# Optimization experiments

Measured on AMD Instinct MI355X. Metric: run time of the kernel, lower is better.

Reference implementation:

```python
import jax, jax.numpy as jnp
import numpy as np

B, T, D = 4, 2048, 1024
H, S = 16, 64  # n_heads, stalk_dim; D == H*S
P_ADIC_BASE = 2
MAX_VAL = 16


def quantize_6bit(x):
    # symmetric int6 quantization with straight-through estimator
    scale = jnp.max(jnp.abs(x)) / 31.0 + 1e-8
    q = jnp.clip(jnp.round(x / scale), -31, 31) * scale
    return x + jax.lax.stop_gradient(q - x)


def build_p_adic_bias(seq_len, p=2, max_val=16):
    idx = jnp.arange(seq_len)
    d = jnp.abs(idx[:, None] - idx[None, :])
    nonzero = d > 0
    vp = jnp.zeros_like(d)
    work = d
    for _ in range(max_val):  # fixed iterations; v_2(|i-j|) <= log2(T) < 16
        divisible = nonzero & (work % p == 0)
        vp = vp + divisible.astype(vp.dtype)
        work = jnp.where(divisible, work // p, work)
    vals = jnp.minimum(vp, max_val).astype(jnp.float32)
    vals = jnp.where(nonzero, vals, jnp.float32(max_val))
    return vals / max_val


def setup_inputs() -> dict:
    key = jax.random.key(0)
    ks = jax.random.split(key, 8)
    std = 0.02
    return {
        "x": jax.random.normal(ks[0], (B, T, D), dtype=jnp.float32),
        "wq": jax.random.normal(ks[1], (D, D), dtype=jnp.float32) * std,
        "wk": jax.random.normal(ks[2], (D, D), dtype=jnp.float32) * std,
        "wv": jax.random.normal(ks[3], (D, D), dtype=jnp.float32) * std,
        "wo": jax.random.normal(ks[4], (D, D), dtype=jnp.float32) * std,
        "wu": jax.random.normal(ks[5], (S, S), dtype=jnp.float32) * std,
        "wsv": jax.random.normal(ks[6], (S, S), dtype=jnp.float32) * std,
        "p_scale": jnp.ones((1,), dtype=jnp.float32) * 0.1,
    }


def reference(x, wq, wk, wv, wo, wu, wsv, p_scale):
    h, s = H, S
    scale = 1.0 / jnp.sqrt(jnp.float32(s))
    # quantized linear projections (F.linear: x @ W.T)
    Q = (x @ quantize_6bit(wq).T).reshape(B, T, h, s).transpose(0, 2, 1, 3)
    K = (x @ quantize_6bit(wk).T).reshape(B, T, h, s).transpose(0, 2, 1, 3)
    V = (x @ quantize_6bit(wv).T).reshape(B, T, h, s).transpose(0, 2, 1, 3)
    # stalk (low-rank sheaf) maps on the head dim
    Qs = Q @ quantize_6bit(wu).T
    Ks = K @ quantize_6bit(wsv).T
    scores = jnp.einsum("bhqs,bhks->bhqk", Qs, Ks) * scale
    p_bias = build_p_adic_bias(T, p=P_ADIC_BASE, max_val=MAX_VAL)
    scores = scores + p_scale[0] * p_bias[None, None, :, :]
    causal = jnp.triu(jnp.ones((T, T), dtype=bool), k=1)
    scores = jnp.where(causal[None, None], -jnp.inf, scores)
    attn = jax.nn.softmax(scores, axis=-1)
    out = jnp.einsum("bhqk,bhks->bhqs", attn, V)
    out = out.transpose(0, 2, 1, 3).reshape(B, T, D)
    return out @ quantize_6bit(wo).T
```

## Files before the change

### kernel.cpp

```cpp
#include <hip/hip_runtime.h>
#include <hip/hip_bf16.h>
#include <stdint.h>


typedef __bf16 bf16_t;
typedef __attribute__((ext_vector_type(4))) __bf16 bf16x4;
typedef __attribute__((ext_vector_type(8))) __bf16 bf16x8;
typedef __attribute__((ext_vector_type(4))) float f32x4;

#define BB 4
#define TT 2048
#define DD 1024
#define HH 16
#define SS 64

__device__ __forceinline__ float quant6(float v, float s) {
    float q = rintf(v / s);
    q = fminf(fmaxf(q, -31.0f), 31.0f);
    return q * s;
}

__device__ __forceinline__ float fexp2(float x) {
#if __has_builtin(__builtin_amdgcn_exp2f)
    return __builtin_amdgcn_exp2f(x);
#else
    return exp2f(x);
#endif
}

typedef __attribute__((address_space(3))) uint32_t lds_u32;
typedef const __attribute__((address_space(1))) uint32_t glb_u32;

__global__ __launch_bounds__(256) void absmax6(const float* __restrict__ wq,
                                               const float* __restrict__ wk,
                                               const float* __restrict__ wv,
                                               const float* __restrict__ wo,
                                               const float* __restrict__ wu,
                                               const float* __restrict__ wsv,
                                               float* __restrict__ amax) {
    const int t = blockIdx.y;
    const float* src = (t == 0) ? wq : (t == 1) ? wk : (t == 2) ? wv
                     : (t == 3) ? wo : (t == 4) ? wu : wsv;
    const int n4 = (t < 4) ? (1048576 / 4) : (4096 / 4);
    float m = 0.0f;
    for (int i = blockIdx.x * blockDim.x + threadIdx.x; i < n4; i += gridDim.x * blockDim.x) {
        float4 v = ((const float4*)src)[i];
        m = fmaxf(m, fmaxf(fmaxf(fabsf(v.x), fabsf(v.y)), fmaxf(fabsf(v.z), fabsf(v.w))));
    }
    #pragma unroll
    for (int mask = 32; mask > 0; mask >>= 1)
        m = fmaxf(m, __shfl_xor(m, mask));
    __shared__ float red[4];
    int w = threadIdx.x >> 6;
    if ((threadIdx.x & 63) == 0) red[w] = m;
    __syncthreads();
    if (threadIdx.x == 0) {
        m = fmaxf(fmaxf(red[0], red[1]), fmaxf(red[2], red[3]));
        atomicMax((int*)(amax + t), __float_as_int(m));
    }
}

__global__ __launch_bounds__(256) void xcvt_kernel(const float* __restrict__ x,
                                                   bf16_t* __restrict__ xb) {
    int i = (blockIdx.x * 256 + threadIdx.x) * 8;
    float4 f0 = *(const float4*)(x + i);
    float4 f1 = *(const float4*)(x + i + 4);
    bf16x8 v;
    v[0] = (bf16_t)f0.x; v[1] = (bf16_t)f0.y; v[2] = (bf16_t)f0.z; v[3] = (bf16_t)f0.w;
    v[4] = (bf16_t)f1.x; v[5] = (bf16_t)f1.y; v[6] = (bf16_t)f1.z; v[7] = (bf16_t)f1.w;
    *(bf16x8*)(xb + i) = v;
}

__global__ __launch_bounds__(256) void prep_w(const float* __restrict__ wq,
                                              const float* __restrict__ wk,
                                              const float* __restrict__ wv,
                                              const float* __restrict__ wo,
                                              const float* __restrict__ wu,
                                              const float* __restrict__ wsv,
                                              const float* __restrict__ amax,
                                              bf16_t* __restrict__ W_all,
                                              bf16_t* __restrict__ Wo) {
    const int which = blockIdx.y;
    if (blockIdx.x < 512) {
        const float* src = which ? wo : wv;
        bf16_t* dst = which ? Wo : (W_all + (size_t)2048 * 1024);
        float s = amax[which ? 3 : 2] / 31.0f + 1e-8f;
        int i = (blockIdx.x * 256 + threadIdx.x) * 8;
        float4 f0 = *(const float4*)(src + i);
        float4 f1 = *(const float4*)(src + i + 4);
        bf16x8 v;
        v[0] = (bf16_t)quant6(f0.x, s); v[1] = (bf16_t)quant6(f0.y, s);
        v[2] = (bf16_t)quant6(f0.z, s); v[3] = (bf16_t)quant6(f0.w, s);
        v[4] = (bf16_t)quant6(f1.x, s); v[5] = (bf16_t)quant6(f1.y, s);
        v[6] = (bf16_t)quant6(f1.z, s); v[7] = (bf16_t)quant6(f1.w, s);
        *(bf16x8*)(dst + i) = v;
        return;
    }
    const int fx = blockIdx.x - 512;
    const float* wbig = which ? wk : wq;
    const float* wsml = which ? wsv : wu;
    const float sb = amax[which ? 1 : 0] / 31.0f + 1e-8f;
    const float ss = amax[which ? 5 : 4] / 31.0f + 1e-8f;
    const float oscale = which ? 1.0f : 0.125f * 1.44269504089f;
    bf16_t* outp = W_all + (size_t)which * 1024 * 1024;
    const int h = fx >> 4, n0 = (fx & 15) * 64;
    const int w = threadIdx.x >> 6, l = threadIdx.x & 63;
    const int l15 = l & 15, quad = l >> 4, q8 = quad * 8;
    const int m0 = w * 16;

    bf16x8 af[2];
    #pragma unroll
    for (int kc = 0; kc < 2; ++kc) {
        const float* src = wsml + (m0 + l15) * 64 + kc * 32 + q8;
        float4 f0 = *(const float4*)(src);
        float4 f1 = *(const float4*)(src + 4);
        bf16x8 a;
        a[0] = (bf16_t)quant6(f0.x, ss); a[1] = (bf16_t)quant6(f0.y, ss);
        a[2] = (bf16_t)quant6(f0.z, ss); a[3] = (bf16_t)quant6(f0.w, ss);
        a[4] = (bf16_t)quant6(f1.x, ss); a[5] = (bf16_t)quant6(f1.y, ss);
        a[6] = (bf16_t)quant6(f1.z, ss); a[7] = (bf16_t)quant6(f1.w, ss);
        af[kc] = a;
    }
    f32x4 acc[4];
    #pragma unroll
    for (int nb = 0; nb < 4; ++nb) acc[nb] = (f32x4){0.f, 0.f, 0.f, 0.f};
    #pragma unroll
    for (int kc = 0; kc < 2; ++kc) {
        #pragma unroll
        for (int nb = 0; nb < 4; ++nb) {
            bf16x8 bfr;
            #pragma unroll
            for (int j = 0; j < 8; ++j)
                bfr[j] = (bf16_t)quant6(wbig[(size_t)(h * 64 + kc * 32 + q8 + j) * 1024 + n0 + nb * 16 + l15], sb);
            acc[nb] = __builtin_amdgcn_mfma_f32_16x16x32_bf16(af[kc], bfr, acc[nb], 0, 0, 0);
        }
    }
    #pragma unroll
    for (int nb = 0; nb < 4; ++nb)
        #pragma unroll
        for (int r = 0; r < 4; ++r)
            outp[(size_t)(h * 64 + m0 + quad * 4 + r) * 1024 + n0 + nb * 16 + l15] =
                (bf16_t)(acc[nb][r] * oscale);
}

template <bool OUT_F32>
__global__ __launch_bounds__(256) void gemm128(const bf16_t* __restrict__ A,
                                               const bf16_t* __restrict__ Bt,
                                               void* __restrict__ Cv,
                                               int lda, int ldb, int ldc, int K) {
    __shared__ __align__(16) bf16_t As[128 * 64];
    __shared__ __align__(16) bf16_t Bs[128 * 64];
    const int tid = threadIdx.x;
    const int w = tid >> 6, l = tid & 63;
    const int l15 = l & 15, quad = l >> 4;
    const int m0 = blockIdx.y * 128, n0 = blockIdx.x * 128;
    const int wm = (w & 1) * 64, wn = (w >> 1) * 64;

    f32x4 acc[4][4];
    #pragma unroll
    for (int a = 0; a < 4; ++a)
        #pragma unroll
        for (int b = 0; b < 4; ++b) acc[a][b] = (f32x4){0.f, 0.f, 0.f, 0.f};

    for (int kc = 0; kc < K; kc += 64) {
        __syncthreads();
        #pragma unroll
        for (int rep = 0; rep < 4; ++rep) {
            int ci = rep * 256 + w * 64 + l;
            int row = ci >> 3, slot = ci & 7;
            int gch = slot ^ ((row ^ (row >> 3)) & 7);
            __builtin_amdgcn_global_load_lds(
                (glb_u32*)(A + (size_t)(m0 + row) * lda + kc + gch * 8),
                (lds_u32*)(As + (rep * 256 + w * 64) * 8), 16, 0, 0);
            __builtin_amdgcn_global_load_lds(
                (glb_u32*)(Bt + (size_t)(n0 + row) * ldb + kc + gch * 8),
                (lds_u32*)(Bs + (rep * 256 + w * 64) * 8), 16, 0, 0);
        }
        __syncthreads();
        #pragma unroll
        for (int kb = 0; kb < 2; ++kb) {
            bf16x8 af[4], bfr[4];
            #pragma unroll
            for (int mb = 0; mb < 4; ++mb) {
                int row = wm + mb * 16 + l15;
                int slot = ((kb << 2) + quad) ^ ((row ^ (row >> 3)) & 7);
                af[mb] = *(const bf16x8*)(As + (row << 6) + slot * 8);
            }
            #pragma unroll
            for (int nb = 0; nb < 4; ++nb) {
                int row = wn + nb * 16 + l15;
                int slot = ((kb << 2) + quad) ^ ((row ^ (row >> 3)) & 7);
                bfr[nb] = *(const bf16x8*)(Bs + (row << 6) + slot * 8);
            }
            #pragma unroll
            for (int mb = 0; mb < 4; ++mb)
                #pragma unroll
                for (int nb = 0; nb < 4; ++nb)
                    acc[mb][nb] = __builtin_amdgcn_mfma_f32_16x16x32_bf16(af[mb], bfr[nb], acc[mb][nb], 0, 0, 0);
        }
    }
    #pragma unroll
    for (int mb = 0; mb < 4; ++mb) {
        #pragma unroll
        for (int nb = 0; nb < 4; ++nb) {
            int col = n0 + wn + nb * 16 + l15;
            #pragma unroll
            for (int r = 0; r < 4; ++r) {
                int row = m0 + wm + mb * 16 + quad * 4 + r;
                if constexpr (OUT_F32)
                    ((float*)Cv)[(size_t)row * ldc + col] = acc[mb][nb][r];
                else
                    ((bf16_t*)Cv)[(size_t)row * ldc + col] = (bf16_t)acc[mb][nb][r];
            }
        }
    }
}

__global__ __launch_bounds__(256) void vtrans_kernel(const bf16_t* __restrict__ QKV,
                                                     bf16_t* __restrict__ Vt) {
    __shared__ __align__(16) bf16_t tile[64 * 72];
    const int tid = threadIdx.x;
    const int bh = blockIdx.x >> 5, tt = blockIdx.x & 31;
    const int b = bh >> 4, h = bh & 15;
    #pragma unroll
    for (int rep = 0; rep < 2; ++rep) {
        int ci = rep * 256 + tid;
        int row = ci >> 3, ch = ci & 7;
        bf16x8 v = *(const bf16x8*)(QKV + ((size_t)(b * TT + tt * 64 + row)) * 3072 + 2048 + h * 64 + ch * 8);
        #pragma unroll
        for (int j = 0; j < 8; ++j) tile[(ch * 8 + j) * 72 + row] = v[j];
    }
    __syncthreads();
    #pragma unroll
    for (int rep = 0; rep < 2; ++rep) {
        int ci = rep * 256 + tid;
        int s = ci >> 3, ch = ci & 7;
        bf16x8 v = *(const bf16x8*)(tile + s * 72 + ch * 8);
        *(bf16x8*)(Vt + ((size_t)(bh * 64 + s)) * TT + tt * 64 + ch * 8) = v;
    }
}

__device__ __forceinline__ void attn_step(bf16_t* __restrict__ Pw,
                                          const bf16x8 kb[4][2], const bf16x8 vb[4][2],
                                          const bf16x8 qa[2],
                                          f32x4* oacc, float& lrun,
                                          int qlane, int kbase, bool diag, float pb2,
                                          int l15, int quad) {
    f32x4 sacc[4];
    #pragma unroll
    for (int c = 0; c < 4; ++c) sacc[c] = (f32x4){0.f, 0.f, 0.f, 0.f};
    #pragma unroll
    for (int kc = 0; kc < 2; ++kc)
        #pragma unroll
        for (int c = 0; c < 4; ++c)
            sacc[c] = __builtin_amdgcn_mfma_f32_16x16x32_bf16(kb[c][kc], qa[kc], sacc[c], 0, 0, 0);

    const int kp0 = kbase + quad * 4;
    #pragma unroll
    for (int c = 0; c < 4; ++c) {
        bf16x4 pk;
        #pragma unroll
        for (int r = 0; r < 4; ++r) {
            const int k = kp0 + c * 16 + r;
            const int d = qlane - k;
            float ctzf = (float)__builtin_ctz((unsigned)d | 0x10000u);
            float s2 = sacc[c][r] + pb2 * ctzf;
            if (diag && k > qlane) s2 = -INFINITY;
            float p = fexp2(s2);
            lrun += p;
            pk[r] = (bf16_t)p;
        }
        int pp = (c * 2 + (quad >> 1)) ^ (l15 & 7);
        *(bf16x4*)(Pw + l15 * 64 + pp * 8 + (quad & 1) * 4) = pk;
    }
    __builtin_amdgcn_wave_barrier();
    #pragma unroll
    for (int kc = 0; kc < 2; ++kc) {
        bf16x8 pa = *(const bf16x8*)(Pw + l15 * 64 + (((kc * 4 + quad) ^ (l15 & 7)) * 8));
        #pragma unroll
        for (int sb = 0; sb < 4; ++sb)
            oacc[sb] = __builtin_amdgcn_mfma_f32_16x16x32_bf16(pa, vb[sb][kc], oacc[sb], 0, 0, 0);
    }
    __builtin_amdgcn_wave_barrier();
}

__global__ __launch_bounds__(256, 2) void attn_kernel(const bf16_t* __restrict__ QKV,
                                                      const bf16_t* __restrict__ Vt,
                                                      const float* __restrict__ p_scale_ptr,
                                                      bf16_t* __restrict__ O) {
    __shared__ __align__(16) bf16_t Ks[64 * 64];
    __shared__ __align__(16) bf16_t Vs[64 * 64];
    __shared__ __align__(16) bf16_t Ps[4 * 16 * 64];

    const int tid = threadIdx.x;
    const int w = tid >> 6, l = tid & 63;
    const int l15 = l & 15, quad = l >> 4, q8 = quad * 8;
    const int pair = (blockIdx.x >> 3) & 15;
    const int bh = (blockIdx.x & 7) + ((blockIdx.x >> 7) << 3);
    const int b = bh >> 4, h = bh & 15;
    const int qtA = pair, qtB = 31 - pair;
    const int q0A = qtA * 64 + w * 16, q0B = qtB * 64 + w * 16;
    const int qlA = q0A + l15, qlB = q0B + l15;

    const float pb2 = p_scale_ptr[0] * 1.44269504089f * 0.0625f;
    const size_t xbase = (size_t)b * TT * 3072;

    bf16x8 qaA[2], qaB[2];
    #pragma unroll
    for (int kc = 0; kc < 2; ++kc) {
        qaA[kc] = *(const bf16x8*)(QKV + xbase + (size_t)(q0A + l15) * 3072 + h * 64 + kc * 32 + q8);
        qaB[kc] = *(const bf16x8*)(QKV + xbase + (size_t)(q0B + l15) * 3072 + h * 64 + kc * 32 + q8);
    }

    f32x4 oA[4], oB[4];
    float lA = 0.f, lB = 0.f;
    #pragma unroll
    for (int i = 0; i < 4; ++i) {
        oA[i] = (f32x4){0.f, 0.f, 0.f, 0.f};
        oB[i] = (f32x4){0.f, 0.f, 0.f, 0.f};
    }
    bf16_t* Pw = Ps + w * 1024;

    for (int kt = 0; kt <= qtB; ++kt) {
        const int kbase = kt * 64;
        __syncthreads();
        #pragma unroll
        for (int rep = 0; rep < 2; ++rep) {
            int ci = rep * 256 + tid;
            int row = ci >> 3, slot = ci & 7;
            int gch = slot ^ ((row ^ (row >> 3)) & 7);
            __builtin_amdgcn_global_load_lds(
                (glb_u32*)(QKV + xbase + (size_t)(kbase + row) * 3072 + 1024 + h * 64 + gch * 8),
                (lds_u32*)(Ks + (rep * 256 + w * 64) * 8), 16, 0, 0);
            __builtin_amdgcn_global_load_lds(
                (glb_u32*)(Vt + (size_t)bh * 131072 + (size_t)row * 2048 + kbase + gch * 8),
                (lds_u32*)(Vs + (rep * 256 + w * 64) * 8), 16, 0, 0);
        }
        __syncthreads();
        bf16x8 kb[4][2], vb[4][2];
        #pragma unroll
        for (int kc = 0; kc < 2; ++kc) {
            #pragma unroll
            for (int c = 0; c < 4; ++c) {
                int row = c * 16 + l15;
                int slot = (kc * 4 + quad) ^ ((row ^ (row >> 3)) & 7);
                kb[c][kc] = *(const bf16x8*)(Ks + row * 64 + slot * 8);
                vb[c][kc] = *(const bf16x8*)(Vs + row * 64 + slot * 8);
            }
        }
        attn_step(Pw, kb, vb, qaB, oB, lB, qlB, kbase, kt == qtB, pb2, l15, quad);
        if (kt <= qtA)
            attn_step(Pw, kb, vb, qaA, oA, lA, qlA, kbase, kt == qtA, pb2, l15, quad);
    }

    #pragma unroll
    for (int t = 0; t < 2; ++t) {
        float s = t ? lB : lA;
        f32x4* oo = t ? oB : oA;
        int q0 = t ? q0B : q0A;
        s += __shfl_xor(s, 16);
        s += __shfl_xor(s, 32);
        float inv = 1.0f / s;
        #pragma unroll
        for (int r = 0; r < 4; ++r) {
            float invr = __shfl(inv, quad * 4 + r);
            #pragma unroll
            for (int sb = 0; sb < 4; ++sb) {
                int q = q0 + quad * 4 + r;
                int col = h * 64 + sb * 16 + l15;
                O[(size_t)(b * TT + q) * DD + col] = (bf16_t)(oo[sb][r] * invr);
            }
        }
    }
}

extern "C" void kernel_launch(void* const* d_in, const int* in_sizes, int n_in,
                              void* d_out, int out_size, void* d_ws, size_t ws_size,
                              hipStream_t stream) {
    const float* x   = (const float*)d_in[0];
    const float* wq  = (const float*)d_in[1];
    const float* wk  = (const float*)d_in[2];
    const float* wv  = (const float*)d_in[3];
    const float* wo  = (const float*)d_in[4];
    const float* wu  = (const float*)d_in[5];
    const float* wsv = (const float*)d_in[6];
    const float* psc = (const float*)d_in[7];
    float* out = (float*)d_out;

    char* ws = (char*)d_ws;
    float*  amax  = (float*)(ws);
    bf16_t* W_all = (bf16_t*)(ws + 256);
    bf16_t* Wo    = (bf16_t*)(ws + 6291712);
    bf16_t* xb    = (bf16_t*)(ws + 8388864);
    bf16_t* Obuf  = xb;
    bf16_t* QKV   = (bf16_t*)(ws + 25166080);
    bf16_t* Vt    = (bf16_t*)(ws + 75497728);

    hipLaunchKernelGGL(absmax6, dim3(64, 6), dim3(256), 0, stream, wq, wk, wv, wo, wu, wsv, amax);
    hipLaunchKernelGGL(prep_w, dim3(768, 2), dim3(256), 0, stream,
                       wq, wk, wv, wo, wu, wsv, amax, W_all, Wo);
    hipLaunchKernelGGL(xcvt_kernel, dim3(4096), dim3(256), 0, stream, x, xb);

    hipLaunchKernelGGL((gemm128<false>), dim3(24, 64), dim3(256), 0, stream,
                       xb, W_all, (void*)QKV, 1024, 1024, 3072, 1024);

    hipLaunchKernelGGL(vtrans_kernel, dim3(2048), dim3(256), 0, stream, QKV, Vt);

    hipLaunchKernelGGL(attn_kernel, dim3(1024), dim3(256), 0, stream, QKV, Vt, psc, Obuf);

    hipLaunchKernelGGL((gemm128<true>), dim3(8, 64), dim3(256), 0, stream,
                       Obuf, Wo, (void*)out, 1024, 1024, 1024, 1024);
}
```

Baseline: 285.5 us.

## Double-buffer K/V tiles in LDS to prefetch next tile during compute

Splits the K and V shared-memory tiles into two buffers and issues the asynchronous global-to-LDS loads for the next key tile before computing on the current one. This is meant to hide global load latency behind the MFMA and softmax work of each attention step. It roughly doubles K/V LDS usage and adds a redundant initial load. The overlap may be lost if the compiler inserts a full vmcnt wait before the current-tile LDS reads.

```diff
diff --git a/kernel.cpp b/kernel.cpp
--- a/kernel.cpp
+++ b/kernel.cpp
@@ -288,8 +288,8 @@
                                                       const bf16_t* __restrict__ Vt,
                                                       const float* __restrict__ p_scale_ptr,
                                                       bf16_t* __restrict__ O) {
-    __shared__ __align__(16) bf16_t Ks[64 * 64];
-    __shared__ __align__(16) bf16_t Vs[64 * 64];
+    __shared__ __align__(16) bf16_t Ks[2][64 * 64];
+    __shared__ __align__(16) bf16_t Vs[2][64 * 64];
     __shared__ __align__(16) bf16_t Ps[4 * 16 * 64];
 
     const int tid = threadIdx.x;
@@ -305,6 +305,13 @@
     const float pb2 = p_scale_ptr[0] * 1.44269504089f * 0.0625f;
     const size_t xbase = (size_t)b * TT * 3072;
 
+    const int srow = tid >> 3, sslot = tid & 7;
+    const int sgch = sslot ^ ((srow ^ (srow >> 3)) & 7);
+    const int srow2 = (tid + 256) >> 3, sslot2 = tid & 7;
+    const int sgch2 = sslot2 ^ ((srow2 ^ (srow2 >> 3)) & 7);
+    const bf16_t* Kg = QKV + xbase + 1024 + h * 64;
+    const bf16_t* Vg = Vt + (size_t)bh * 131072;
+
     bf16x8 qaA[2], qaB[2];
     #pragma unroll
     for (int kc = 0; kc < 2; ++kc) {
@@ -321,22 +328,47 @@
     }
     bf16_t* Pw = Ps + w * 1024;
 
-    for (int kt = 0; kt <= qtB; ++kt) {
-        const int kbase = kt * 64;
-        __syncthreads();
+    {
+        const int kbase = 0;
+        __builtin_amdgcn_global_load_lds((glb_u32*)(Kg + (size_t)(kbase + srow) * 3072 + sgch * 8),
+                                         (lds_u32*)(Ks[0] + (tid >> 3) * 64 + 0), 16, 0, 0);
+    }
+
+    {
         #pragma unroll
         for (int rep = 0; rep < 2; ++rep) {
             int ci = rep * 256 + tid;
             int row = ci >> 3, slot = ci & 7;
             int gch = slot ^ ((row ^ (row >> 3)) & 7);
             __builtin_amdgcn_global_load_lds(
-                (glb_u32*)(QKV + xbase + (size_t)(kbase + row) * 3072 + 1024 + h * 64 + gch * 8),
-                (lds_u32*)(Ks + (rep * 256 + w * 64) * 8), 16, 0, 0);
+                (glb_u32*)(Kg + (size_t)row * 3072 + gch * 8),
+                (lds_u32*)(Ks[0] + (rep * 256 + w * 64) * 8), 16, 0, 0);
             __builtin_amdgcn_global_load_lds(
-                (glb_u32*)(Vt + (size_t)bh * 131072 + (size_t)row * 2048 + kbase + gch * 8),
-                (lds_u32*)(Vs + (rep * 256 + w * 64) * 8), 16, 0, 0);
-        }
+                (glb_u32*)(Vg + (size_t)row * 2048 + gch * 8),
+                (lds_u32*)(Vs[0] + (rep * 256 + w * 64) * 8), 16, 0, 0);
+        }
+    }
+
+    for (int kt = 0; kt <= qtB; ++kt) {
+        const int cur = kt & 1;
         __syncthreads();
+        if (kt < qtB) {
+            const int kbase1 = (kt + 1) * 64;
+            const int nxt = cur ^ 1;
+            #pragma unroll
+            for (int rep = 0; rep < 2; ++rep) {
+                int ci = rep * 256 + tid;
+                int row = ci >> 3, slot = ci & 7;
+                int gch = slot ^ ((row ^ (row >> 3)) & 7);
+                __builtin_amdgcn_global_load_lds(
+                    (glb_u32*)(Kg + (size_t)(kbase1 + row) * 3072 + gch * 8),
+                    (lds_u32*)(Ks[nxt] + (rep * 256 + w * 64) * 8), 16, 0, 0);
+                __builtin_amdgcn_global_load_lds(
+                    (glb_u32*)(Vg + (size_t)row * 2048 + kbase1 + gch * 8),
+                    (lds_u32*)(Vs[nxt] + (rep * 256 + w * 64) * 8), 16, 0, 0);
+            }
+        }
+        const int kbase = kt * 64;
         bf16x8 kb[4][2], vb[4][2];
         #pragma unroll
         for (int kc = 0; kc < 2; ++kc) {
@@ -344,8 +376,8 @@
             for (int c = 0; c < 4; ++c) {
                 int row = c * 16 + l15;
                 int slot = (kc * 4 + quad) ^ ((row ^ (row >> 3)) & 7);
-                kb[c][kc] = *(const bf16x8*)(Ks + row * 64 + slot * 8);
-                vb[c][kc] = *(const bf16x8*)(Vs + row * 64 + slot * 8);
+                kb[c][kc] = *(const bf16x8*)(Ks[cur] + row * 64 + slot * 8);
+                vb[c][kc] = *(const bf16x8*)(Vs[cur] + row * 64 + slot * 8);
             }
         }
         attn_step(Pw, kb, vb, qaB, oB, lB, qlB, kbase, kt == qtB, pb2, l15, quad);
```

After: 290.8 us. Within noise of the previous version (+1.9%).

## Assign each wave to one query tile with two row-slices instead of both tiles

Applied to the files above, without the earlier changes.

Waves 0-1 now handle the long query tile (qtB) and waves 2-3 handle the short one (qtA), each wave covering 32 rows as two 16-row slices, where before every wave did 16 rows of both tiles. This lets the K/V fragments read from LDS be reused for two row-slices of the same tile. The cost is load imbalance: waves on the short tile sit idle at barriers for later key tiles while the other two waves work, so per-block latency is set by the long tile done by only half the waves.

```diff
diff --git a/kernel.cpp b/kernel.cpp
--- a/kernel.cpp
+++ b/kernel.cpp
@@ -299,26 +299,28 @@
     const int bh = (blockIdx.x & 7) + ((blockIdx.x >> 7) << 3);
     const int b = bh >> 4, h = bh & 15;
     const int qtA = pair, qtB = 31 - pair;
-    const int q0A = qtA * 64 + w * 16, q0B = qtB * 64 + w * 16;
-    const int qlA = q0A + l15, qlB = q0B + l15;
+    const int myqt = (w < 2) ? qtB : qtA;
+    const int qrow0 = myqt * 64 + (w & 1) * 32;
 
     const float pb2 = p_scale_ptr[0] * 1.44269504089f * 0.0625f;
     const size_t xbase = (size_t)b * TT * 3072;
-
-    bf16x8 qaA[2], qaB[2];
-    #pragma unroll
-    for (int kc = 0; kc < 2; ++kc) {
-        qaA[kc] = *(const bf16x8*)(QKV + xbase + (size_t)(q0A + l15) * 3072 + h * 64 + kc * 32 + q8);
-        qaB[kc] = *(const bf16x8*)(QKV + xbase + (size_t)(q0B + l15) * 3072 + h * 64 + kc * 32 + q8);
-    }
-
-    f32x4 oA[4], oB[4];
-    float lA = 0.f, lB = 0.f;
-    #pragma unroll
-    for (int i = 0; i < 4; ++i) {
-        oA[i] = (f32x4){0.f, 0.f, 0.f, 0.f};
-        oB[i] = (f32x4){0.f, 0.f, 0.f, 0.f};
-    }
+    const bf16_t* Kg = QKV + xbase + 1024 + h * 64;
+    const bf16_t* Vg = Vt + (size_t)bh * 131072;
+
+    bf16x8 qa[2][2];
+    #pragma unroll
+    for (int rs = 0; rs < 2; ++rs)
+        #pragma unroll
+        for (int kc = 0; kc < 2; ++kc)
+            qa[rs][kc] = *(const bf16x8*)(QKV + xbase +
+                (size_t)(qrow0 + rs * 16 + l15) * 3072 + h * 64 + kc * 32 + q8);
+
+    f32x4 oacc[2][4];
+    float lr[2] = {0.f, 0.f};
+    #pragma unroll
+    for (int rs = 0; rs < 2; ++rs)
+        #pragma unroll
+        for (int i = 0; i < 4; ++i) oacc[rs][i] = (f32x4){0.f, 0.f, 0.f, 0.f};
     bf16_t* Pw = Ps + w * 1024;
 
     for (int kt = 0; kt <= qtB; ++kt) {
@@ -330,34 +332,37 @@
             int row = ci >> 3, slot = ci & 7;
             int gch = slot ^ ((row ^ (row >> 3)) & 7);
             __builtin_amdgcn_global_load_lds(
-                (glb_u32*)(QKV + xbase + (size_t)(kbase + row) * 3072 + 1024 + h * 64 + gch * 8),
+                (glb_u32*)(Kg + (size_t)(kbase + row) * 3072 + gch * 8),
                 (lds_u32*)(Ks + (rep * 256 + w * 64) * 8), 16, 0, 0);
             __builtin_amdgcn_global_load_lds(
-                (glb_u32*)(Vt + (size_t)bh * 131072 + (size_t)row * 2048 + kbase + gch * 8),
+                (glb_u32*)(Vg + (size_t)row * 2048 + kbase + gch * 8),
                 (lds_u32*)(Vs + (rep * 256 + w * 64) * 8), 16, 0, 0);
         }
         __syncthreads();
-        bf16x8 kb[4][2], vb[4][2];
-        #pragma unroll
-        for (int kc = 0; kc < 2; ++kc) {
-            #pragma unroll
-            for (int c = 0; c < 4; ++c) {
-                int row = c * 16 + l15;
-                int slot = (kc * 4 + quad) ^ ((row ^ (row >> 3)) & 7);
-                kb[c][kc] = *(const bf16x8*)(Ks + row * 64 + slot * 8);
-                vb[c][kc] = *(const bf16x8*)(Vs + row * 64 + slot * 8);
+        if (kt <= myqt) {
+            bf16x8 kb[4][2], vb[4][2];
+            #pragma unroll
+            for (int kc = 0; kc < 2; ++kc) {
+                #pragma unroll
+                for (int c = 0; c < 4; ++c) {
+                    int row = c * 16 + l15;
+                    int slot = (kc * 4 + quad) ^ ((row ^ (row >> 3)) & 7);
+                    kb[c][kc] = *(const bf16x8*)(Ks + row * 64 + slot * 8);
+                    vb[c][kc] = *(const bf16x8*)(Vs + row * 64 + slot * 8);
+                }
             }
-        }
-        attn_step(Pw, kb, vb, qaB, oB, lB, qlB, kbase, kt == qtB, pb2, l15, quad);
-        if (kt <= qtA)
-            attn_step(Pw, kb, vb, qaA, oA, lA, qlA, kbase, kt == qtA, pb2, l15, quad);
-    }
-
-    #pragma unroll
-    for (int t = 0; t < 2; ++t) {
-        float s = t ? lB : lA;
-        f32x4* oo = t ? oB : oA;
-        int q0 = t ? q0B : q0A;
+            #pragma unroll
+            for (int rs = 0; rs < 2; ++rs)
+                attn_step(Pw, kb, vb, qa[rs], oacc[rs], lr[rs],
+                          qrow0 + rs * 16 + l15, kbase, kt == myqt, pb2, l15, quad);
+        }
+    }
+
+    #pragma unroll
+    for (int rs = 0; rs < 2; ++rs) {
+        float s = lr[rs];
+        f32x4* oo = oacc[rs];
+        int q0 = qrow0 + rs * 16;
         s += __shfl_xor(s, 16);
         s += __shfl_xor(s, 32);
         float inv = 1.0f / s;
```

Result: slower. 321.1 us (+12.5%).
